# Kernel tuning notes

Measured on AMD Instinct MI355X. Metric: run time of the kernel, lower is better.

Reference implementation:

```python
import jax, jax.numpy as jnp
import numpy as np

N = 500          # number of gaussians (hardcoded loop bound in source)
H = W = 1024     # fixed raster grid in source


def setup_inputs() -> dict:
    key = jax.random.key(0)
    k1, k2, k3 = jax.random.split(key, 3)
    # means in pixel coordinates
    mean = jax.random.uniform(k1, (N, 2), dtype=jnp.float32, minval=0.0, maxval=1023.0)
    # depth as produced by __init__: clamp(x/2.5 + 0.6, 0.1, 1) * 10  -> in [1, 10]
    depth = jnp.clip(jax.random.normal(k2, (N,), dtype=jnp.float32) / 2.5 + 0.6, 0.1, 1.0) * 10.0
    # radii is a log-std; scaled O(1) so splats cover multiple pixels
    radii = jnp.abs(jax.random.normal(k3, (N,), dtype=jnp.float32)) * 1.5 + 0.5
    # fixed red color per gaussian, as in __init__
    color = jnp.tile(jnp.array([255.0, 0.0, 0.0], dtype=jnp.float32), (N, 1))
    return {"mean": mean, "depth": depth, "radii": radii, "color": color}


def reference(mean, depth, radii, color):
    # torch.meshgrid default is 'ij' indexing
    xx, yy = jnp.meshgrid(jnp.arange(H, dtype=jnp.float32),
                          jnp.arange(W, dtype=jnp.float32), indexing="ij")
    two_pi = jnp.float32(2.0 * np.pi)

    def body(acc, p):
        m, d, r, c = p  # m:[2], d:[], r:[], c:[3]
        # rotated coords simplify: xx_rot - m0 = xx - yy + m1 - m0 ; yy_rot - m1 = xx + yy - m0 - m1
        u = xx - yy + (m[1] - m[0])
        v = xx + yy - (m[0] + m[1])
        inv_var = jnp.exp(-2.0 * r)  # 1 / exp(2*log_std)
        # normalizer uses exp(r/2)*exp(r/2) = exp(r) as in the source
        g = d * jnp.exp(-0.5 * (u * u + v * v) * inv_var) / (two_pi * jnp.exp(r))
        return acc + c[:, None, None] * g, None

    acc0 = jnp.zeros((3, H, W), dtype=jnp.float32)
    out, _ = jax.lax.scan(body, acc0, (mean, depth, radii, color))
    return out
```

## Files before the change

kernel.cpp:

```cpp
#include <hip/hip_runtime.h>
#include <math.h>

#define HH 1024
#define WW 1024
#define TILE 32
#define NTX (WW / TILE)
#define NTY (HH / TILE)
#define ROWS_PER_THREAD 4
#define THREADS 256
#define MAXG 1024


__global__ __launch_bounds__(256) void gauss_prep(
    const float* __restrict__ mean, const float* __restrict__ depth,
    const float* __restrict__ radii, const float* __restrict__ color,
    float* __restrict__ params, int n) {
  int g = blockIdx.x * blockDim.x + threadIdx.x;
  if (g >= n) return;
  float m0 = mean[2 * g + 0];
  float m1 = mean[2 * g + 1];
  float d  = depth[g];
  float r  = radii[g];

  const float LOG2E = 1.4426950408889634f;
  const float TWO_PI = 6.283185307179586f;

  float A = m1 - m0;
  float B = m0 + m1;
  float sig2inv = __expf(-2.0f * r);
  float iv2 = -0.5f * LOG2E * sig2inv;
  float norm = d / (TWO_PI * __expf(r));
  float w0 = color[3 * g + 0] * norm;
  float w1 = color[3 * g + 1] * norm;
  float w2 = color[3 * g + 2] * norm;
  float wmax = fmaxf(fabsf(w0), fmaxf(fabsf(w1), fabsf(w2)));
  float R2 = 2.0f * logf(wmax * 1e5f + 1e-30f) * __expf(2.0f * r);

  float* p = params + 8 * g;
  p[0] = A;  p[1] = B;  p[2] = iv2; p[3] = R2;
  p[4] = w0; p[5] = w1; p[6] = w2;  p[7] = 0.0f;
}

__global__ __launch_bounds__(THREADS) void gauss_raster(
    const float* __restrict__ params, float* __restrict__ out, int n) {
  __shared__ int s_count;
  __shared__ int s_list[MAXG];

  const int tile_x = blockIdx.x % NTX;
  const int tile_y = blockIdx.x / NTX;
  const int j0 = tile_x * TILE;
  const int i0 = tile_y * TILE;

  if (threadIdx.x == 0) s_count = 0;
  __syncthreads();

  for (int g = threadIdx.x; g < n; g += THREADS) {
    const float* p = params + 8 * g;
    float A = p[0], B = p[1], R2 = p[3];
    float u_lo = (float)(i0 - (j0 + TILE - 1)) + A;
    float u_hi = (float)(i0 + TILE - 1 - j0) + A;
    float v_lo = (float)(i0 + j0) - B;
    float v_hi = (float)(i0 + TILE - 1 + j0 + TILE - 1) - B;
    float du = fmaxf(0.0f, fmaxf(u_lo, -u_hi));
    float dv = fmaxf(0.0f, fmaxf(v_lo, -v_hi));
    if (du * du + dv * dv <= R2) {
      int idx = atomicAdd(&s_count, 1);
      if (idx < MAXG) s_list[idx] = g;
    }
  }
  __syncthreads();
  int cnt = s_count;
  if (cnt > MAXG) cnt = MAXG;

  const int jj = threadIdx.x % TILE;
  const int ib = (threadIdx.x / TILE) * ROWS_PER_THREAD;
  const int i_glob = i0 + ib;
  const int j_glob = j0 + jj;

  const float t1 = (float)(i_glob - j_glob);
  const float t2 = (float)(i_glob + j_glob);

  float acc[ROWS_PER_THREAD][3];
#pragma unroll
  for (int di = 0; di < ROWS_PER_THREAD; ++di) {
    acc[di][0] = 0.0f; acc[di][1] = 0.0f; acc[di][2] = 0.0f;
  }

  for (int k = 0; k < cnt; ++k) {
    int g = __builtin_amdgcn_readfirstlane(s_list[k]);
    const float* p = params + 8 * g;
    float A = p[0], B = p[1], iv2 = p[2];
    float w0 = p[4], w1 = p[5], w2 = p[6];
    float ub = t1 + A;
    float vb = t2 - B;
#pragma unroll
    for (int di = 0; di < ROWS_PER_THREAD; ++di) {
      float u = ub + (float)di;
      float v = vb + (float)di;
      float t = fmaf(u, u, v * v);
      float e = exp2f(t * iv2);
      acc[di][0] = fmaf(w0, e, acc[di][0]);
      acc[di][1] = fmaf(w1, e, acc[di][1]);
      acc[di][2] = fmaf(w2, e, acc[di][2]);
    }
  }

#pragma unroll
  for (int c = 0; c < 3; ++c) {
#pragma unroll
    for (int di = 0; di < ROWS_PER_THREAD; ++di) {
      out[c * (HH * WW) + (i_glob + di) * WW + j_glob] = acc[di][c];
    }
  }
}

extern "C" void kernel_launch(void* const* d_in, const int* in_sizes, int n_in,
                              void* d_out, int out_size, void* d_ws, size_t ws_size,
                              hipStream_t stream) {
  const float* mean  = (const float*)d_in[0];
  const float* depth = (const float*)d_in[1];
  const float* radii = (const float*)d_in[2];
  const float* color = (const float*)d_in[3];
  float* out = (float*)d_out;
  float* params = (float*)d_ws;
  int n = in_sizes[1];

  gauss_prep<<<(n + 255) / 256, 256, 0, stream>>>(mean, depth, radii, color,
                                                  params, n);
  gauss_raster<<<dim3(NTX * NTY), THREADS, 0, stream>>>(params, out, n);
}
```

Before: 71.63 us.

## Prescale gaussian params, cache culled list in LDS, use smaller tiles with single-channel fast path

Gaussian coordinates are prescaled by sqrt of the inverse variance, so each pixel evaluation needs two FMAs, one squared-sum and a raw exp2. The culling radius becomes a log2 threshold. Per-tile culled parameters are copied into shared memory instead of being re-read from global memory. Tiles shrink to 32x8 with one pixel per thread, which gives more blocks. A runtime flag skips the green and blue accumulation when all culled weights for those channels are zero, which cuts FMA and LDS traffic for the red-only inputs. The trade-offs are the loss of per-thread row reuse and that MAXG is halved to 512.

```diff
diff --git a/kernel.cpp b/kernel.cpp
--- a/kernel.cpp
+++ b/kernel.cpp
@@ -3,12 +3,12 @@
 
 #define HH 1024
 #define WW 1024
-#define TILE 32
-#define NTX (WW / TILE)
-#define NTY (HH / TILE)
-#define ROWS_PER_THREAD 4
+#define TW 32
+#define TH 8
+#define NTX (WW / TW)
+#define NTY (HH / TH)
 #define THREADS 256
-#define MAXG 1024
+#define MAXG 512
 
 
 __global__ __launch_bounds__(256) void gauss_prep(
@@ -25,93 +25,99 @@
   const float LOG2E = 1.4426950408889634f;
   const float TWO_PI = 6.283185307179586f;
 
-  float A = m1 - m0;
-  float B = m0 + m1;
-  float sig2inv = __expf(-2.0f * r);
-  float iv2 = -0.5f * LOG2E * sig2inv;
+  float q = 0.5f * LOG2E * __expf(-2.0f * r);
+  float s = sqrtf(q);
+  float As  = (m1 - m0) * s;
+  float Bsn = -(m0 + m1) * s;
   float norm = d / (TWO_PI * __expf(r));
   float w0 = color[3 * g + 0] * norm;
   float w1 = color[3 * g + 1] * norm;
   float w2 = color[3 * g + 2] * norm;
   float wmax = fmaxf(fabsf(w0), fmaxf(fabsf(w1), fabsf(w2)));
-  float R2 = 2.0f * logf(wmax * 1e5f + 1e-30f) * __expf(2.0f * r);
+  float R2s = __log2f(wmax * 1e5f);
 
   float* p = params + 8 * g;
-  p[0] = A;  p[1] = B;  p[2] = iv2; p[3] = R2;
+  p[0] = s;  p[1] = As; p[2] = Bsn; p[3] = R2s;
   p[4] = w0; p[5] = w1; p[6] = w2;  p[7] = 0.0f;
 }
 
 __global__ __launch_bounds__(THREADS) void gauss_raster(
-    const float* __restrict__ params, float* __restrict__ out, int n) {
+    const float4* __restrict__ params, float* __restrict__ out, int n) {
   __shared__ int s_count;
-  __shared__ int s_list[MAXG];
+  __shared__ int s_flag;
+  __shared__ float4 s_pa[MAXG];
+  __shared__ float2 s_pb[MAXG];
 
   const int tile_x = blockIdx.x % NTX;
   const int tile_y = blockIdx.x / NTX;
-  const int j0 = tile_x * TILE;
-  const int i0 = tile_y * TILE;
+  const int j0 = tile_x * TW;
+  const int i0 = tile_y * TH;
 
-  if (threadIdx.x == 0) s_count = 0;
+  if (threadIdx.x == 0) { s_count = 0; s_flag = 0; }
   __syncthreads();
 
   for (int g = threadIdx.x; g < n; g += THREADS) {
-    const float* p = params + 8 * g;
-    float A = p[0], B = p[1], R2 = p[3];
-    float u_lo = (float)(i0 - (j0 + TILE - 1)) + A;
-    float u_hi = (float)(i0 + TILE - 1 - j0) + A;
-    float v_lo = (float)(i0 + j0) - B;
-    float v_hi = (float)(i0 + TILE - 1 + j0 + TILE - 1) - B;
-    float du = fmaxf(0.0f, fmaxf(u_lo, -u_hi));
-    float dv = fmaxf(0.0f, fmaxf(v_lo, -v_hi));
-    if (du * du + dv * dv <= R2) {
+    float4 pa = params[2 * g + 0];
+    float4 pb = params[2 * g + 1];
+    float s = pa.x, As = pa.y, Bsn = pa.z, R2s = pa.w;
+    float ul = fmaf(s, (float)(i0 - (j0 + TW - 1)), As);
+    float uh = fmaf(s, (float)(i0 + TH - 1 - j0), As);
+    float vl = fmaf(s, (float)(i0 + j0), Bsn);
+    float vh = fmaf(s, (float)(i0 + TH - 1 + j0 + TW - 1), Bsn);
+    float du = fmaxf(0.0f, fmaxf(ul, -uh));
+    float dv = fmaxf(0.0f, fmaxf(vl, -vh));
+    if (fmaf(du, du, dv * dv) <= R2s) {
       int idx = atomicAdd(&s_count, 1);
-      if (idx < MAXG) s_list[idx] = g;
+      if (idx < MAXG) {
+        s_pa[idx] = make_float4(s, As, Bsn, pb.x);
+        s_pb[idx] = make_float2(pb.y, pb.z);
+        if (pb.y != 0.0f || pb.z != 0.0f) s_flag = 1;
+      }
     }
   }
   __syncthreads();
   int cnt = s_count;
   if (cnt > MAXG) cnt = MAXG;
+  const int rgb = s_flag;
 
-  const int jj = threadIdx.x % TILE;
-  const int ib = (threadIdx.x / TILE) * ROWS_PER_THREAD;
-  const int i_glob = i0 + ib;
+  const int jj = threadIdx.x & (TW - 1);
+  const int ii = threadIdx.x >> 5;
+  const int i_glob = i0 + ii;
   const int j_glob = j0 + jj;
-
   const float t1 = (float)(i_glob - j_glob);
   const float t2 = (float)(i_glob + j_glob);
 
-  float acc[ROWS_PER_THREAD][3];
-#pragma unroll
-  for (int di = 0; di < ROWS_PER_THREAD; ++di) {
-    acc[di][0] = 0.0f; acc[di][1] = 0.0f; acc[di][2] = 0.0f;
-  }
+  float a0 = 0.0f, a1 = 0.0f, a2 = 0.0f;
 
-  for (int k = 0; k < cnt; ++k) {
-    int g = __builtin_amdgcn_readfirstlane(s_list[k]);
-    const float* p = params + 8 * g;
-    float A = p[0], B = p[1], iv2 = p[2];
-    float w0 = p[4], w1 = p[5], w2 = p[6];
-    float ub = t1 + A;
-    float vb = t2 - B;
-#pragma unroll
-    for (int di = 0; di < ROWS_PER_THREAD; ++di) {
-      float u = ub + (float)di;
-      float v = vb + (float)di;
-      float t = fmaf(u, u, v * v);
-      float e = exp2f(t * iv2);
-      acc[di][0] = fmaf(w0, e, acc[di][0]);
-      acc[di][1] = fmaf(w1, e, acc[di][1]);
-      acc[di][2] = fmaf(w2, e, acc[di][2]);
+  if (!rgb) {
+#pragma unroll 4
+    for (int k = 0; k < cnt; ++k) {
+      float4 pa = s_pa[k];
+      float u = fmaf(t1, pa.x, pa.y);
+      float v = fmaf(t2, pa.x, pa.z);
+      float t = fmaf(v, v, u * u);
+      float e = __builtin_amdgcn_exp2f(-t);
+      a0 = fmaf(pa.w, e, a0);
+    }
+  } else {
+#pragma unroll 4
+    for (int k = 0; k < cnt; ++k) {
+      float4 pa = s_pa[k];
+      float2 pb = s_pb[k];
+      float u = fmaf(t1, pa.x, pa.y);
+      float v = fmaf(t2, pa.x, pa.z);
+      float t = fmaf(v, v, u * u);
+      float e = __builtin_amdgcn_exp2f(-t);
+      a0 = fmaf(pa.w, e, a0);
+      a1 = fmaf(pb.x, e, a1);
+      a2 = fmaf(pb.y, e, a2);
     }
   }
 
-#pragma unroll
-  for (int c = 0; c < 3; ++c) {
-#pragma unroll
-    for (int di = 0; di < ROWS_PER_THREAD; ++di) {
-      out[c * (HH * WW) + (i_glob + di) * WW + j_glob] = acc[di][c];
-    }
-  }
+  const int base = i_glob * WW + j_glob;
+  out[0 * (HH * WW) + base] = a0;
+  out[1 * (HH * WW) + base] = a1;
+  out[2 * (HH * WW) + base] = a2;
 }
 
 extern "C" void kernel_launch(void* const* d_in, const int* in_sizes, int n_in,
@@ -127,5 +133,6 @@
 
   gauss_prep<<<(n + 255) / 256, 256, 0, stream>>>(mean, depth, radii, color,
                                                   params, n);
-  gauss_raster<<<dim3(NTX * NTY), THREADS, 0, stream>>>(params, out, n);
+  gauss_raster<<<dim3(NTX * NTY), THREADS, 0, stream>>>(
+      (const float4*)params, out, n);
 }
```

Result: faster. 67.69 us (-5.5%).
